# Kernel optimization log

Measured on AMD Instinct MI355X. Metric: run time of the kernel, lower is better.

The kernel has to match this reference:

```python
import jax, jax.numpy as jnp
import numpy as np

HIDDEN = 512
ATT_DIM = 128
LN_EPS = 1e-3  # keras LayerNormalization default epsilon


def setup_inputs() -> dict:
    key = jax.random.key(0)
    k1, k2, k3, k4 = jax.random.split(key, 4)
    hidden_states = jax.random.normal(k1, (64, 2048, HIDDEN), dtype=jnp.float32)
    # Glorot-uniform style init for the dense weights
    def glorot(k, shape):
        lim = np.sqrt(6.0 / (shape[0] + shape[1]))
        return jax.random.uniform(k, shape, jnp.float32, -lim, lim)
    W_a = glorot(k2, (HIDDEN, ATT_DIM))
    U_a = glorot(k3, (HIDDEN, ATT_DIM))
    v_a = glorot(k4, (ATT_DIM, 1))
    ln_gamma = jnp.ones((HIDDEN,), jnp.float32)
    ln_beta = jnp.zeros((HIDDEN,), jnp.float32)
    return {"hidden_states": hidden_states, "W_a": W_a, "U_a": U_a,
            "v_a": v_a, "ln_gamma": ln_gamma, "ln_beta": ln_beta}


def reference(hidden_states, W_a, U_a, v_a, ln_gamma, ln_beta):
    # hidden_states: (B, L, H)
    h_att = jnp.einsum('blh,ha->bla', hidden_states, W_a)        # (B, L, A)
    context = jnp.mean(hidden_states, axis=1, keepdims=True)     # (B, 1, H)
    u_att = jnp.einsum('blh,ha->bla', context, U_a)              # (B, 1, A) broadcasts
    combined = jnp.tanh(h_att + u_att)                           # (B, L, A)
    scores = jnp.einsum('bla,ao->bl', combined, v_a)             # (B, L)
    attn = jax.nn.softmax(scores, axis=-1)                       # (B, L)
    attended = jnp.einsum('blh,bl->bh', hidden_states, attn)     # (B, H)
    # LayerNormalization over last axis
    mu = jnp.mean(attended, axis=-1, keepdims=True)
    var = jnp.var(attended, axis=-1, keepdims=True)
    normed = (attended - mu) * jax.lax.rsqrt(var + LN_EPS)
    out = normed * ln_gamma + ln_beta
    return out, attn
```

## Files before the change

kernel.cpp:

```cpp
#include <hip/hip_runtime.h>
#include <hip/hip_bf16.h>

#define HIDDEN 512
#define ATT    128
#define NB     64
#define SL     2048
#define LN_EPS 1e-3f

typedef __attribute__((ext_vector_type(8))) short short8;
typedef __attribute__((ext_vector_type(4))) short short4v;
typedef __attribute__((ext_vector_type(4))) float f32x4;

__device__ __forceinline__ short f2bf(float f) {
    union { float f; unsigned u; } v; v.f = f;
    unsigned r = v.u + 0x7fffu + ((v.u >> 16) & 1u);
    return (short)(r >> 16);
}
__device__ __forceinline__ float bf2f(short b) {
    union { unsigned u; float f; } v;
    v.u = ((unsigned)(unsigned short)b) << 16; return v.f;
}
__device__ __forceinline__ float tanh_fast(float x) {
    float cx = fminf(fmaxf(x, -15.f), 15.f);
    float e = __expf(2.f * cx);
    return (e - 1.f) * __builtin_amdgcn_rcpf(e + 1.f);
}

__launch_bounds__(256)
__global__ void p1_gemm_ctx(const float* __restrict__ hidden, const float* __restrict__ W,
                            short* __restrict__ h_att, float* __restrict__ ctx_part) {
    __shared__ char smem[32768];
    short* As    = (short*)smem;
    short* Ws    = (short*)(smem + 8192);
    float* ctx_s = (float*)(smem + 16384);
    short* out_s = (short*)smem;

    int t = threadIdx.x;
    int row0 = blockIdx.x * 128;
    int wave = t >> 6, lane = t & 63, quad = lane >> 4, cb = lane & 15;

    ctx_s[t] = 0.f; ctx_s[t + 256] = 0.f;

    f32x4 acc[2][8];
    #pragma unroll
    for (int mt = 0; mt < 2; ++mt)
        #pragma unroll
        for (int nt = 0; nt < 8; ++nt)
            acc[mt][nt] = (f32x4){0.f, 0.f, 0.f, 0.f};

    for (int k0 = 0; k0 < HIDDEN; k0 += 32) {
        __syncthreads();
        float cx = 0.f, cy = 0.f, cz = 0.f, cw = 0.f;
        #pragma unroll
        for (int it = 0; it < 4; ++it) {
            int f = t + it * 256;
            int row = f >> 3, kpos = (f & 7) * 4;
            const float4 g = *(const float4*)(hidden + ((size_t)(row0 + row)) * HIDDEN + k0 + kpos);
            cx += g.x; cy += g.y; cz += g.z; cw += g.w;
            short4v s4 = { f2bf(g.x), f2bf(g.y), f2bf(g.z), f2bf(g.w) };
            *(short4v*)(&As[row * 32 + kpos]) = s4;
        }
        #pragma unroll
        for (int it = 0; it < 4; ++it) {
            int k = (t >> 5) + it * 8;
            int n4 = (t & 31) * 4;
            const float4 g = *(const float4*)(W + (k0 + k) * ATT + n4);
            Ws[(n4 + 0) * 32 + k] = f2bf(g.x);
            Ws[(n4 + 1) * 32 + k] = f2bf(g.y);
            Ws[(n4 + 2) * 32 + k] = f2bf(g.z);
            Ws[(n4 + 3) * 32 + k] = f2bf(g.w);
        }
        __syncthreads();
        cx += __shfl_xor(cx, 8);  cy += __shfl_xor(cy, 8);  cz += __shfl_xor(cz, 8);  cw += __shfl_xor(cw, 8);
        cx += __shfl_xor(cx, 16); cy += __shfl_xor(cy, 16); cz += __shfl_xor(cz, 16); cw += __shfl_xor(cw, 16);
        cx += __shfl_xor(cx, 32); cy += __shfl_xor(cy, 32); cz += __shfl_xor(cz, 32); cw += __shfl_xor(cw, 32);
        if (lane < 8) {
            atomicAdd(&ctx_s[k0 + lane * 4 + 0], cx);
            atomicAdd(&ctx_s[k0 + lane * 4 + 1], cy);
            atomicAdd(&ctx_s[k0 + lane * 4 + 2], cz);
            atomicAdd(&ctx_s[k0 + lane * 4 + 3], cw);
        }
        short8 a0 = *(const short8*)(&As[(wave * 32 + cb) * 32 + quad * 8]);
        short8 a1 = *(const short8*)(&As[(wave * 32 + 16 + cb) * 32 + quad * 8]);
        #pragma unroll
        for (int nt = 0; nt < 8; ++nt) {
            short8 bf = *(const short8*)(&Ws[(nt * 16 + cb) * 32 + quad * 8]);
            acc[0][nt] = __builtin_amdgcn_mfma_f32_16x16x32_bf16(a0, bf, acc[0][nt], 0, 0, 0);
            acc[1][nt] = __builtin_amdgcn_mfma_f32_16x16x32_bf16(a1, bf, acc[1][nt], 0, 0, 0);
        }
    }
    __syncthreads();
    ctx_part[(size_t)blockIdx.x * HIDDEN + t]       = ctx_s[t];
    ctx_part[(size_t)blockIdx.x * HIDDEN + 256 + t] = ctx_s[t + 256];
    __syncthreads();
    #pragma unroll
    for (int mt = 0; mt < 2; ++mt)
        #pragma unroll
        for (int nt = 0; nt < 8; ++nt)
            #pragma unroll
            for (int j = 0; j < 4; ++j)
                out_s[(wave * 32 + mt * 16 + quad * 4 + j) * 128 + nt * 16 + cb] = f2bf(acc[mt][nt][j]);
    __syncthreads();
    short8* dst = (short8*)(h_att + (size_t)row0 * ATT);
    const short8* src = (const short8*)out_s;
    #pragma unroll
    for (int i = 0; i < 8; ++i) dst[t + i * 256] = src[t + i * 256];
}

__launch_bounds__(256)
__global__ void p2_uatt(const float* __restrict__ ctx_part, const float* __restrict__ U,
                        float* __restrict__ uatt) {
    int b = blockIdx.x, t = threadIdx.x;
    __shared__ float cs[HIDDEN];
    float s0 = 0.f, s1 = 0.f;
    #pragma unroll
    for (int c = 0; c < 16; ++c) {
        size_t base = (size_t)(b * 16 + c) * HIDDEN;
        s0 += ctx_part[base + t];
        s1 += ctx_part[base + 256 + t];
    }
    cs[t] = s0; cs[t + 256] = s1;
    __syncthreads();
    if (t < ATT) {
        float d = 0.f;
        #pragma unroll 8
        for (int h = 0; h < HIDDEN; ++h) d += cs[h] * U[h * ATT + t];
        uatt[b * ATT + t] = d * (1.f / SL);
    }
}

__launch_bounds__(256)
__global__ void p3_scores(const short* __restrict__ h_att, const float* __restrict__ v_a,
                          const float* __restrict__ uatt, float* __restrict__ scores) {
    int t = threadIdx.x, bx = blockIdx.x;
    int row0 = bx * 64, b = bx >> 5;
    __shared__ float v_s[ATT], u_s[ATT];
    if (t < ATT) { v_s[t] = v_a[t]; u_s[t] = uatt[b * ATT + t]; }
    __syncthreads();
    int lr = t >> 2, seg = t & 3;
    const short8* p = (const short8*)(h_att + ((size_t)(row0 + lr)) * ATT + seg * 32);
    float s = 0.f;
    #pragma unroll
    for (int q = 0; q < 4; ++q) {
        short8 h8 = p[q];
        #pragma unroll
        for (int i = 0; i < 8; ++i) {
            int a = seg * 32 + q * 8 + i;
            s += v_s[a] * tanh_fast(bf2f(h8[i]) + u_s[a]);
        }
    }
    s += __shfl_xor(s, 1);
    s += __shfl_xor(s, 2);
    if (seg == 0) scores[row0 + lr] = s;
}

__launch_bounds__(256)
__global__ void p4_softmax(float* __restrict__ attn) {
    int b = blockIdx.x, t = threadIdx.x;
    float* p = attn + b * SL;
    __shared__ float red[256];
    float v[8];
    float m = -1e30f;
    #pragma unroll
    for (int i = 0; i < 8; ++i) { v[i] = p[t + i * 256]; m = fmaxf(m, v[i]); }
    red[t] = m; __syncthreads();
    for (int s = 128; s > 0; s >>= 1) { if (t < s) red[t] = fmaxf(red[t], red[t + s]); __syncthreads(); }
    m = red[0]; __syncthreads();
    float sum = 0.f;
    #pragma unroll
    for (int i = 0; i < 8; ++i) { v[i] = __expf(v[i] - m); sum += v[i]; }
    red[t] = sum; __syncthreads();
    for (int s = 128; s > 0; s >>= 1) { if (t < s) red[t] += red[t + s]; __syncthreads(); }
    float inv = 1.f / red[0];
    #pragma unroll
    for (int i = 0; i < 8; ++i) p[t + i * 256] = v[i] * inv;
}

__launch_bounds__(256)
__global__ void p5_attended(const float* __restrict__ hidden, const float* __restrict__ attn,
                            float* __restrict__ att_part) {
    int b = blockIdx.y, c = blockIdx.x, t = threadIdx.x;
    __shared__ float w_s[128];
    __shared__ float4 red_s[128];
    if (t < 128) w_s[t] = attn[b * SL + c * 128 + t];
    __syncthreads();
    int cg = t & 127, half = t >> 7;
    const float* hp = hidden + ((size_t)b * SL + c * 128 + half * 64) * HIDDEN + cg * 4;
    float4 a = {0.f, 0.f, 0.f, 0.f};
    #pragma unroll 4
    for (int l = 0; l < 64; ++l) {
        float w = w_s[half * 64 + l];
        const float4 g = *(const float4*)(hp + (size_t)l * HIDDEN);
        a.x += w * g.x; a.y += w * g.y; a.z += w * g.z; a.w += w * g.w;
    }
    if (half) red_s[cg] = a;
    __syncthreads();
    if (!half) {
        float4 r = red_s[cg];
        a.x += r.x; a.y += r.y; a.z += r.z; a.w += r.w;
        *(float4*)(att_part + ((size_t)(c * NB + b)) * HIDDEN + cg * 4) = a;
    }
}

__launch_bounds__(256)
__global__ void p6_ln(const float* __restrict__ att_part, const float* __restrict__ gamma,
                      const float* __restrict__ beta, float* __restrict__ out) {
    int b = blockIdx.x, t = threadIdx.x;
    float x0 = 0.f, x1 = 0.f;
    #pragma unroll
    for (int c = 0; c < 16; ++c) {
        size_t base = (size_t)(c * NB + b) * HIDDEN;
        x0 += att_part[base + t];
        x1 += att_part[base + t + 256];
    }
    __shared__ float rs[256], rq[256];
    rs[t] = x0 + x1; rq[t] = x0 * x0 + x1 * x1;
    __syncthreads();
    for (int s = 128; s > 0; s >>= 1) {
        if (t < s) { rs[t] += rs[t + s]; rq[t] += rq[t + s]; }
        __syncthreads();
    }
    float mean = rs[0] * (1.f / HIDDEN);
    float var = rq[0] * (1.f / HIDDEN) - mean * mean;
    float r = rsqrtf(var + LN_EPS);
    out[b * HIDDEN + t]       = (x0 - mean) * r * gamma[t] + beta[t];
    out[b * HIDDEN + t + 256] = (x1 - mean) * r * gamma[t + 256] + beta[t + 256];
}

extern "C" void kernel_launch(void* const* d_in, const int* in_sizes, int n_in,
                              void* d_out, int out_size, void* d_ws, size_t ws_size,
                              hipStream_t stream) {
    const float* hidden = (const float*)d_in[0];
    const float* W      = (const float*)d_in[1];
    const float* U      = (const float*)d_in[2];
    const float* v_a    = (const float*)d_in[3];
    const float* gamma  = (const float*)d_in[4];
    const float* beta   = (const float*)d_in[5];

    float* out  = (float*)d_out;
    float* attn = out + NB * HIDDEN;

    short* h_att    = (short*)d_ws;
    float* ctx_part = (float*)((char*)d_ws + (size_t)NB * SL * ATT * 2);
    float* att_part = ctx_part + (size_t)1024 * HIDDEN;
    float* uatt     = att_part + (size_t)16 * NB * HIDDEN;

    p1_gemm_ctx<<<(NB * SL) / 128, 256, 0, stream>>>(hidden, W, h_att, ctx_part);
    p2_uatt<<<NB, 256, 0, stream>>>(ctx_part, U, uatt);
    p3_scores<<<(NB * SL) / 64, 256, 0, stream>>>(h_att, v_a, uatt, attn);
    p4_softmax<<<NB, 256, 0, stream>>>(attn);
    p5_attended<<<dim3(16, NB), 256, 0, stream>>>(hidden, attn, att_part);
    p6_ln<<<NB, 256, 0, stream>>>(att_part, gamma, beta, out);
}
```

Baseline: 527.3 us.

## Pre-transpose W to bf16 and load GEMM operands directly into registers

Adds a small kernel that converts W to a transposed bf16 copy once per call. The main GEMM kernel then reads A rows and bf16 W columns straight from global memory into MFMA operand registers, dropping the per-k-step LDS staging and both block barriers. The context column sums are reduced with shuffles across the 16 row lanes. The output staging buffer is padded to 136 columns to reduce LDS bank conflicts. The trade-offs are an extra kernel launch, less coalesced global reads (each lane reads 32 bytes from a different row), and repeated W reads served from cache.

```diff
diff --git a/kernel.cpp b/kernel.cpp
--- a/kernel.cpp
+++ b/kernel.cpp
@@ -26,20 +26,24 @@
     return (e - 1.f) * __builtin_amdgcn_rcpf(e + 1.f);
 }
 
-__launch_bounds__(256)
-__global__ void p1_gemm_ctx(const float* __restrict__ hidden, const float* __restrict__ W,
+__global__ void p0_wt(const float* __restrict__ W, short* __restrict__ Wt) {
+    int idx = blockIdx.x * 256 + threadIdx.x;
+    int a = idx >> 9, h = idx & 511;
+    Wt[idx] = f2bf(W[h * ATT + a]);
+}
+
+__launch_bounds__(256)
+__global__ void p1_gemm_ctx(const float* __restrict__ hidden, const short* __restrict__ Wt,
                             short* __restrict__ h_att, float* __restrict__ ctx_part) {
-    __shared__ char smem[32768];
-    short* As    = (short*)smem;
-    short* Ws    = (short*)(smem + 8192);
-    float* ctx_s = (float*)(smem + 16384);
-    short* out_s = (short*)smem;
+    __shared__ float ctx_s[HIDDEN];
+    __shared__ short out_s[128 * 136];
 
     int t = threadIdx.x;
     int row0 = blockIdx.x * 128;
     int wave = t >> 6, lane = t & 63, quad = lane >> 4, cb = lane & 15;
 
     ctx_s[t] = 0.f; ctx_s[t + 256] = 0.f;
+    __syncthreads();
 
     f32x4 acc[2][8];
     #pragma unroll
@@ -48,63 +52,66 @@
         for (int nt = 0; nt < 8; ++nt)
             acc[mt][nt] = (f32x4){0.f, 0.f, 0.f, 0.f};
 
+    const float* aptr0 = hidden + (size_t)(row0 + wave * 32 + cb) * HIDDEN;
+    const float* aptr1 = aptr0 + (size_t)16 * HIDDEN;
+    const short* bptr  = Wt + (size_t)cb * HIDDEN;
+
     for (int k0 = 0; k0 < HIDDEN; k0 += 32) {
-        __syncthreads();
-        float cx = 0.f, cy = 0.f, cz = 0.f, cw = 0.f;
-        #pragma unroll
-        for (int it = 0; it < 4; ++it) {
-            int f = t + it * 256;
-            int row = f >> 3, kpos = (f & 7) * 4;
-            const float4 g = *(const float4*)(hidden + ((size_t)(row0 + row)) * HIDDEN + k0 + kpos);
-            cx += g.x; cy += g.y; cz += g.z; cw += g.w;
-            short4v s4 = { f2bf(g.x), f2bf(g.y), f2bf(g.z), f2bf(g.w) };
-            *(short4v*)(&As[row * 32 + kpos]) = s4;
-        }
-        #pragma unroll
-        for (int it = 0; it < 4; ++it) {
-            int k = (t >> 5) + it * 8;
-            int n4 = (t & 31) * 4;
-            const float4 g = *(const float4*)(W + (k0 + k) * ATT + n4);
-            Ws[(n4 + 0) * 32 + k] = f2bf(g.x);
-            Ws[(n4 + 1) * 32 + k] = f2bf(g.y);
-            Ws[(n4 + 2) * 32 + k] = f2bf(g.z);
-            Ws[(n4 + 3) * 32 + k] = f2bf(g.w);
-        }
-        __syncthreads();
-        cx += __shfl_xor(cx, 8);  cy += __shfl_xor(cy, 8);  cz += __shfl_xor(cz, 8);  cw += __shfl_xor(cw, 8);
-        cx += __shfl_xor(cx, 16); cy += __shfl_xor(cy, 16); cz += __shfl_xor(cz, 16); cw += __shfl_xor(cw, 16);
-        cx += __shfl_xor(cx, 32); cy += __shfl_xor(cy, 32); cz += __shfl_xor(cz, 32); cw += __shfl_xor(cw, 32);
-        if (lane < 8) {
-            atomicAdd(&ctx_s[k0 + lane * 4 + 0], cx);
-            atomicAdd(&ctx_s[k0 + lane * 4 + 1], cy);
-            atomicAdd(&ctx_s[k0 + lane * 4 + 2], cz);
-            atomicAdd(&ctx_s[k0 + lane * 4 + 3], cw);
-        }
-        short8 a0 = *(const short8*)(&As[(wave * 32 + cb) * 32 + quad * 8]);
-        short8 a1 = *(const short8*)(&As[(wave * 32 + 16 + cb) * 32 + quad * 8]);
+        int ka = k0 + quad * 8;
+        const float4 a0lo = *(const float4*)(aptr0 + ka);
+        const float4 a0hi = *(const float4*)(aptr0 + ka + 4);
+        const float4 a1lo = *(const float4*)(aptr1 + ka);
+        const float4 a1hi = *(const float4*)(aptr1 + ka + 4);
+
+        short8 b8[8];
+        #pragma unroll
+        for (int nt = 0; nt < 8; ++nt)
+            b8[nt] = *(const short8*)(bptr + nt * 16 * HIDDEN + ka);
+
+        float s[8] = { a0lo.x + a1lo.x, a0lo.y + a1lo.y, a0lo.z + a1lo.z, a0lo.w + a1lo.w,
+                       a0hi.x + a1hi.x, a0hi.y + a1hi.y, a0hi.z + a1hi.z, a0hi.w + a1hi.w };
+        #pragma unroll
+        for (int j = 0; j < 8; ++j) {
+            s[j] += __shfl_xor(s[j], 1);
+            s[j] += __shfl_xor(s[j], 2);
+            s[j] += __shfl_xor(s[j], 4);
+            s[j] += __shfl_xor(s[j], 8);
+        }
+        if (cb == 0) {
+            #pragma unroll
+            for (int j = 0; j < 8; ++j) atomicAdd(&ctx_s[ka + j], s[j]);
+        }
+
+        short8 a0 = { f2bf(a0lo.x), f2bf(a0lo.y), f2bf(a0lo.z), f2bf(a0lo.w),
+                      f2bf(a0hi.x), f2bf(a0hi.y), f2bf(a0hi.z), f2bf(a0hi.w) };
+        short8 a1 = { f2bf(a1lo.x), f2bf(a1lo.y), f2bf(a1lo.z), f2bf(a1lo.w),
+                      f2bf(a1hi.x), f2bf(a1hi.y), f2bf(a1hi.z), f2bf(a1hi.w) };
+
         #pragma unroll
         for (int nt = 0; nt < 8; ++nt) {
-            short8 bf = *(const short8*)(&Ws[(nt * 16 + cb) * 32 + quad * 8]);
-            acc[0][nt] = __builtin_amdgcn_mfma_f32_16x16x32_bf16(a0, bf, acc[0][nt], 0, 0, 0);
-            acc[1][nt] = __builtin_amdgcn_mfma_f32_16x16x32_bf16(a1, bf, acc[1][nt], 0, 0, 0);
+            acc[0][nt] = __builtin_amdgcn_mfma_f32_16x16x32_bf16(a0, b8[nt], acc[0][nt], 0, 0, 0);
+            acc[1][nt] = __builtin_amdgcn_mfma_f32_16x16x32_bf16(a1, b8[nt], acc[1][nt], 0, 0, 0);
         }
     }
     __syncthreads();
     ctx_part[(size_t)blockIdx.x * HIDDEN + t]       = ctx_s[t];
     ctx_part[(size_t)blockIdx.x * HIDDEN + 256 + t] = ctx_s[t + 256];
-    __syncthreads();
+
     #pragma unroll
     for (int mt = 0; mt < 2; ++mt)
         #pragma unroll
         for (int nt = 0; nt < 8; ++nt)
             #pragma unroll
             for (int j = 0; j < 4; ++j)
-                out_s[(wave * 32 + mt * 16 + quad * 4 + j) * 128 + nt * 16 + cb] = f2bf(acc[mt][nt][j]);
-    __syncthreads();
-    short8* dst = (short8*)(h_att + (size_t)row0 * ATT);
-    const short8* src = (const short8*)out_s;
-    #pragma unroll
-    for (int i = 0; i < 8; ++i) dst[t + i * 256] = src[t + i * 256];
+                out_s[(wave * 32 + mt * 16 + quad * 4 + j) * 136 + nt * 16 + cb] = f2bf(acc[mt][nt][j]);
+    __syncthreads();
+    {
+        int row = t >> 1, seg = t & 1;
+        const short* srcp = out_s + row * 136 + seg * 64;
+        short8* dstp = (short8*)(h_att + ((size_t)(row0 + row)) * ATT + seg * 64);
+        #pragma unroll
+        for (int i = 0; i < 8; ++i) dstp[i] = *(const short8*)(srcp + i * 8);
+    }
 }
 
 __launch_bounds__(256)
@@ -244,8 +251,10 @@
     float* ctx_part = (float*)((char*)d_ws + (size_t)NB * SL * ATT * 2);
     float* att_part = ctx_part + (size_t)1024 * HIDDEN;
     float* uatt     = att_part + (size_t)16 * NB * HIDDEN;
-
-    p1_gemm_ctx<<<(NB * SL) / 128, 256, 0, stream>>>(hidden, W, h_att, ctx_part);
+    short* Wt       = (short*)(uatt + NB * ATT);
+
+    p0_wt<<<256, 256, 0, stream>>>(W, Wt);
+    p1_gemm_ctx<<<(NB * SL) / 128, 256, 0, stream>>>(hidden, Wt, h_att, ctx_part);
     p2_uatt<<<NB, 256, 0, stream>>>(ctx_part, U, uatt);
     p3_scores<<<(NB * SL) / 64, 256, 0, stream>>>(h_att, v_a, uatt, attn);
     p4_softmax<<<NB, 256, 0, stream>>>(attn);
```

Measured after the change: 498.0 us. 5.6% less time.
